# Performance work log

Hardware: AMD Instinct MI355X
Metric: run time of the kernel (lower is better)

## Reference

```python
import jax, jax.numpy as jnp
import numpy as np

B, L, E, H = 32, 2048, 512, 512


def setup_inputs() -> dict:
    key = jax.random.key(0)
    k1, k2, k3, k4 = jax.random.split(key, 4)
    encodings = jax.random.normal(k1, (B, L, E), dtype=jnp.float32)
    lengths = jax.random.randint(k2, (B,), 1, L + 1, dtype=jnp.int32)
    # Glorot-ish scaled params
    W_h = jax.random.normal(k3, (E, H), dtype=jnp.float32) / np.sqrt(E)
    b_h = jnp.zeros((H,), dtype=jnp.float32)
    W_c = jax.random.normal(k4, (H, E), dtype=jnp.float32) / np.sqrt(H)
    return {"encodings": encodings, "lengths": lengths, "W_h": W_h, "b_h": b_h, "W_c": W_c}


def reference(encodings, lengths, W_h, b_h, W_c):
    # encodings: [B, L, E] padded ragged pack; lengths: [B] valid lengths
    mask = jnp.arange(encodings.shape[1])[None, :] < lengths[:, None]  # [B, L]
    # hidden_layer with tanh nonlinearity (TimeDistributedLinear)
    h = jnp.tanh(jnp.einsum('ble,eh->blh', encodings, W_h) + b_h)  # [B, L, H]
    # context_vector (no bias) -> per-feature attention logits [B, L, E]
    att = jnp.einsum('blh,he->ble', h, W_c)
    # timedistributed_softmax: softmax over time axis per sample, per feature
    att = jnp.where(mask[:, :, None], att, -jnp.inf)
    att = jax.nn.softmax(att, axis=1)  # padded positions get weight 0
    # weighted sum over time -> [B, E], then unsqueeze(1)
    out = jnp.sum(att * encodings, axis=1)[:, None, :]  # [B, 1, E]
    return out
```

## Files before the change

kernel.cpp:

```cpp
#include <hip/hip_runtime.h>
#include <math.h>

#define BB 32
#define LL 2048
#define EE 512
#define HH 512

typedef __bf16 bf16_t;
typedef bf16_t bf16x8 __attribute__((ext_vector_type(8)));
typedef float f32x4 __attribute__((ext_vector_type(4)));
typedef unsigned short u16x8 __attribute__((ext_vector_type(8)));

__device__ __forceinline__ unsigned short f2bf(float f) {
  unsigned int u = __builtin_bit_cast(unsigned int, f);
  unsigned int r = (u + 0x7FFFu + ((u >> 16) & 1u)) >> 16;
  return (unsigned short)r;
}
__device__ __forceinline__ float bf2f(unsigned short s) {
  unsigned int u = ((unsigned int)s) << 16;
  return __builtin_bit_cast(float, u);
}
__device__ __forceinline__ bf16x8 ld_frag(const unsigned short* p) {
  u16x8 raw = *(const u16x8*)p;
  return __builtin_bit_cast(bf16x8, raw);
}
__device__ __forceinline__ float tanh_fast(float x) {
  x = fminf(fmaxf(x, -15.f), 15.f);
  float e2 = __expf(2.f * x);
  return (e2 - 1.f) / (e2 + 1.f);
}

__device__ __forceinline__ void frag_issue2(const unsigned short* __restrict__ g,
                                            int k0, bf16x8 f[2]) {
#pragma unroll
  for (int i = 0; i < 2; i++) f[i] = ld_frag(g + (size_t)i * 16 * 512 + k0);
}

#define G1_HALF(F, W, PF) do {                                                  \
    const int k0_ = (((W) + phase) & 15) * 32;                                  \
    const bf16x8 b0_ = ld_frag(&encA[(l15     ) * 520 + k0_ + quad * 8]);       \
    const bf16x8 b1_ = ld_frag(&encA[(16 + l15) * 520 + k0_ + quad * 8]);       \
    const bf16x8 b2_ = ld_frag(&encA[(32 + l15) * 520 + k0_ + quad * 8]);       \
    const bf16x8 b3_ = ld_frag(&encA[(48 + l15) * 520 + k0_ + quad * 8]);       \
    _Pragma("unroll")                                                           \
    for (int t_ = 0; t_ < 2; t_++) {                                            \
      acc[t_ * 4 + 0] = __builtin_amdgcn_mfma_f32_16x16x32_bf16(F[t_], b0_, acc[t_ * 4 + 0], 0, 0, 0); \
      acc[t_ * 4 + 1] = __builtin_amdgcn_mfma_f32_16x16x32_bf16(F[t_], b1_, acc[t_ * 4 + 1], 0, 0, 0); \
      acc[t_ * 4 + 2] = __builtin_amdgcn_mfma_f32_16x16x32_bf16(F[t_], b2_, acc[t_ * 4 + 2], 0, 0, 0); \
      acc[t_ * 4 + 3] = __builtin_amdgcn_mfma_f32_16x16x32_bf16(F[t_], b3_, acc[t_ * 4 + 3], 0, 0, 0); \
    }                                                                           \
    if (PF) frag_issue2(baseW, (((W) + 2 + phase) & 15) * 32, F);               \
  } while (0)

#define G2_HALF(F, W, PF) do {                                                  \
    const int k0_ = (((W) + phase) & 15) * 32;                                  \
    const bf16x8 a0_ = ld_frag(&hS[(l15     ) * 520 + k0_ + quad * 8]);         \
    const bf16x8 a1_ = ld_frag(&hS[(16 + l15) * 520 + k0_ + quad * 8]);         \
    const bf16x8 a2_ = ld_frag(&hS[(32 + l15) * 520 + k0_ + quad * 8]);         \
    const bf16x8 a3_ = ld_frag(&hS[(48 + l15) * 520 + k0_ + quad * 8]);         \
    _Pragma("unroll")                                                           \
    for (int e_ = 0; e_ < 2; e_++) {                                            \
      acc[0 * 2 + e_] = __builtin_amdgcn_mfma_f32_16x16x32_bf16(a0_, F[e_], acc[0 * 2 + e_], 0, 0, 0); \
      acc[1 * 2 + e_] = __builtin_amdgcn_mfma_f32_16x16x32_bf16(a1_, F[e_], acc[1 * 2 + e_], 0, 0, 0); \
      acc[2 * 2 + e_] = __builtin_amdgcn_mfma_f32_16x16x32_bf16(a2_, F[e_], acc[2 * 2 + e_], 0, 0, 0); \
      acc[3 * 2 + e_] = __builtin_amdgcn_mfma_f32_16x16x32_bf16(a3_, F[e_], acc[3 * 2 + e_], 0, 0, 0); \
    }                                                                           \
    if (PF) frag_issue2(baseW, (((W) + 2 + phase) & 15) * 32, F);               \
  } while (0)

__global__ __launch_bounds__(256) void prep_w(
    const float* __restrict__ Wh, const float* __restrict__ Wc,
    unsigned short* __restrict__ WhT, unsigned short* __restrict__ WcT,
    int* __restrict__ q)
{
  if (blockIdx.x == 0 && blockIdx.y == 0 && threadIdx.x == 0) *q = 0;
  const float* src = blockIdx.y ? Wc : Wh;
  unsigned short* dst = blockIdx.y ? WcT : WhT;
  const int tr = (blockIdx.x >> 3) * 64;
  const int tc = (blockIdx.x & 7) * 64;
  const int tid = threadIdx.x;
  __shared__ float tile[64][65];
  for (int i = tid; i < 64 * 16; i += 256) {
    const int r = i >> 4, c4 = (i & 15) << 2;
    const float4 v = *(const float4*)(src + (size_t)(tr + r) * 512 + tc + c4);
    tile[r][c4 + 0] = v.x; tile[r][c4 + 1] = v.y;
    tile[r][c4 + 2] = v.z; tile[r][c4 + 3] = v.w;
  }
  __syncthreads();
  for (int i = tid; i < 64 * 16; i += 256) {
    const int r = i >> 4, c4 = (i & 15) << 2;
    ushort4 pk;
    pk.x = f2bf(tile[c4 + 0][r]); pk.y = f2bf(tile[c4 + 1][r]);
    pk.z = f2bf(tile[c4 + 2][r]); pk.w = f2bf(tile[c4 + 3][r]);
    *(ushort4*)(dst + (size_t)(tc + r) * 512 + tr + c4) = pk;
  }
}

__global__ __launch_bounds__(1024, 1) void attn_main(
    const float* __restrict__ enc, const int* __restrict__ lens,
    const unsigned short* __restrict__ WhT, const float* __restrict__ bh,
    const unsigned short* __restrict__ WcT,
    float* __restrict__ pm, float* __restrict__ ps, float* __restrict__ po,
    int* __restrict__ q, int C, int Lc)
{
  const int tid  = threadIdx.x;
  const int lane = tid & 63;
  const int wave = tid >> 6;
  const int quad = lane >> 4;
  const int l15  = lane & 15;
  const int wbase = wave * 32;

  __shared__ __align__(16) unsigned short encA[64 * 520];
  __shared__ __align__(16) unsigned short hS[64 * 520];
  __shared__ __align__(16) float bhS[512];
  __shared__ int itemS;

  if (tid < 512) bhS[tid] = bh[tid];
  const int nitems = 32 * C;

#pragma unroll 1
  for (;;) {
    __syncthreads();
    if (tid == 0) itemS = atomicAdd(q, 1);
    __syncthreads();
    const int item = itemS;
    if (item >= nitems) break;
    const int b = item & 31;
    const int c = item >> 5;
    const int n = lens[b];
    const int l0 = c * Lc;
    const int nvalid = min(n - l0, Lc);
    if (nvalid <= 0) continue;

    const int phase = (item + wave) & 15;

    float stM[2], stS[2], stO[2];
#pragma unroll
    for (int et = 0; et < 2; et++) { stM[et] = -1e30f; stS[et] = 0.f; stO[et] = 0.f; }

    f32x4 acc[8];

#pragma unroll 1
    for (int r0 = 0; r0 < nvalid; r0 += 64) {
      const float* encRow = enc + ((size_t)b * LL + l0 + r0) * EE;
      for (int i = tid; i < 64 * 128; i += 1024) {
        const int m = i >> 7, e4 = (i & 127) << 2;
        const float4 v = *(const float4*)(encRow + (size_t)m * EE + e4);
        ushort4 pk;
        pk.x = f2bf(v.x); pk.y = f2bf(v.y); pk.z = f2bf(v.z); pk.w = f2bf(v.w);
        *(ushort4*)&encA[m * 520 + e4] = pk;
      }
      __syncthreads();

#pragma unroll
      for (int i = 0; i < 8; i++) acc[i] = (f32x4){0.f, 0.f, 0.f, 0.f};
      {
        const unsigned short* baseW = WhT + (size_t)(wbase + l15) * 512 + quad * 8;
        bf16x8 fA[2], fB[2];
        frag_issue2(baseW, ((0 + phase) & 15) * 32, fA);
        frag_issue2(baseW, ((1 + phase) & 15) * 32, fB);
#pragma unroll 1
        for (int kk = 0; kk < 16; kk += 2) {
          G1_HALF(fA, kk + 0, (kk + 2 < 16));
          G1_HALF(fB, kk + 1, (kk + 3 < 16));
        }
      }

#pragma unroll
      for (int t = 0; t < 2; t++) {
        const f32x4 bv = *(const f32x4*)&bhS[wbase + t * 16 + quad * 4];
#pragma unroll
        for (int mt = 0; mt < 4; mt++) {
          ushort4 pk;
          pk.x = f2bf(tanh_fast(acc[t * 4 + mt][0] + bv[0]));
          pk.y = f2bf(tanh_fast(acc[t * 4 + mt][1] + bv[1]));
          pk.z = f2bf(tanh_fast(acc[t * 4 + mt][2] + bv[2]));
          pk.w = f2bf(tanh_fast(acc[t * 4 + mt][3] + bv[3]));
          *(ushort4*)&hS[(mt * 16 + l15) * 520 + wbase + t * 16 + quad * 4] = pk;
        }
      }
      __syncthreads();

#pragma unroll
      for (int i = 0; i < 8; i++) acc[i] = (f32x4){0.f, 0.f, 0.f, 0.f};
      {
        const unsigned short* baseW = WcT + (size_t)(wbase + l15) * 512 + quad * 8;
        bf16x8 fA[2], fB[2];
        frag_issue2(baseW, ((0 + phase) & 15) * 32, fA);
        frag_issue2(baseW, ((1 + phase) & 15) * 32, fB);
#pragma unroll 1
        for (int kk = 0; kk < 16; kk += 2) {
          G2_HALF(fA, kk + 0, (kk + 2 < 16));
          G2_HALF(fB, kk + 1, (kk + 3 < 16));
        }
      }

#pragma unroll
      for (int et = 0; et < 2; et++) {
        const int e = wbase + et * 16 + l15;
        float lm = -1e30f;
#pragma unroll
        for (int mt = 0; mt < 4; mt++)
#pragma unroll
          for (int r = 0; r < 4; r++) {
            const float vv = (r0 + mt * 16 + quad * 4 + r) < nvalid ? acc[mt * 2 + et][r] : -1e30f;
            lm = fmaxf(lm, vv);
          }
        lm = fmaxf(lm, __shfl_xor(lm, 16));
        lm = fmaxf(lm, __shfl_xor(lm, 32));
        float ls = 0.f, lo = 0.f;
#pragma unroll
        for (int mt = 0; mt < 4; mt++)
#pragma unroll
          for (int r = 0; r < 4; r++) {
            const float vv = (r0 + mt * 16 + quad * 4 + r) < nvalid ? acc[mt * 2 + et][r] : -1e30f;
            const float p  = __expf(vv - lm);
            const float ev = bf2f(encA[(mt * 16 + quad * 4 + r) * 520 + e]);
            ls += p;
            lo += p * ev;
          }
        ls += __shfl_xor(ls, 16); ls += __shfl_xor(ls, 32);
        lo += __shfl_xor(lo, 16); lo += __shfl_xor(lo, 32);
        const float Mn = fmaxf(stM[et], lm);
        const float sc = __expf(stM[et] - Mn);
        const float st = __expf(lm - Mn);
        stS[et] = stS[et] * sc + ls * st;
        stO[et] = stO[et] * sc + lo * st;
        stM[et] = Mn;
      }
      __syncthreads();
    }

    if (quad == 0) {
      const size_t base = ((size_t)b * C + c) * EE;
#pragma unroll
      for (int et = 0; et < 2; et++) {
        const int e = wbase + et * 16 + l15;
        pm[base + e] = stM[et];
        ps[base + e] = stS[et];
        po[base + e] = stO[et];
      }
    }
  }
}

__global__ __launch_bounds__(256) void attn_combine(
    const float* __restrict__ pm, const float* __restrict__ ps,
    const float* __restrict__ po, const int* __restrict__ lens,
    float* __restrict__ out, int C, int Lc)
{
  const int b  = blockIdx.y;
  const int e  = blockIdx.x * 64 + (threadIdx.x & 63);
  const int g  = threadIdx.x >> 6;
  const int n  = lens[b];
  const int cmax = min(C, (n + Lc - 1) / Lc);

  float M = -1e30f, S = 0.f, O = 0.f;
  for (int c = g; c < cmax; c += 4) {
    const size_t base = ((size_t)b * C + c) * EE;
    const float m = pm[base + e];
    const float s = ps[base + e];
    const float o = po[base + e];
    const float Mn  = fmaxf(M, m);
    const float sc0 = __expf(M - Mn);
    const float sc1 = __expf(m - Mn);
    S = S * sc0 + s * sc1;
    O = O * sc0 + o * sc1;
    M = Mn;
  }

  __shared__ float sM[4][64], sS[4][64], sO[4][64];
  sM[g][threadIdx.x & 63] = M;
  sS[g][threadIdx.x & 63] = S;
  sO[g][threadIdx.x & 63] = O;
  __syncthreads();

  if (g == 0) {
    const int le = threadIdx.x & 63;
    float Mt = sM[0][le], St = sS[0][le], Ot = sO[0][le];
#pragma unroll
    for (int gg = 1; gg < 4; gg++) {
      const float m = sM[gg][le];
      const float Mn  = fmaxf(Mt, m);
      const float sc0 = __expf(Mt - Mn);
      const float sc1 = __expf(m - Mn);
      St = St * sc0 + sS[gg][le] * sc1;
      Ot = Ot * sc0 + sO[gg][le] * sc1;
      Mt = Mn;
    }
    out[(size_t)b * EE + e] = Ot / St;
  }
}

extern "C" void kernel_launch(void* const* d_in, const int* in_sizes, int n_in,
                              void* d_out, int out_size, void* d_ws, size_t ws_size,
                              hipStream_t stream) {
  const float* enc  = (const float*)d_in[0];
  const int*   lens = (const int*)d_in[1];
  const float* Wh   = (const float*)d_in[2];
  const float* bh   = (const float*)d_in[3];
  const float* Wc   = (const float*)d_in[4];
  float* out = (float*)d_out;

  const size_t wbytes = (size_t)512 * 512 * sizeof(unsigned short);
  int C = 32;
  while (C > 8 && ws_size < (size_t)3 * BB * C * EE * sizeof(float) + 2 * wbytes + 64)
    C >>= 1;
  const int Lc = LL / C;

  float* pm = (float*)d_ws;
  float* ps = pm + (size_t)BB * C * EE;
  float* po = ps + (size_t)BB * C * EE;
  unsigned short* WhT = (unsigned short*)(po + (size_t)BB * C * EE);
  unsigned short* WcT = WhT + (size_t)512 * 512;
  int* q = (int*)(WcT + (size_t)512 * 512);

  prep_w<<<dim3(64, 2), 256, 0, stream>>>(Wh, Wc, WhT, WcT, q);
  attn_main<<<dim3(256), 1024, 0, stream>>>(enc, lens, WhT, bh, WcT, pm, ps, po, q, C, Lc);
  attn_combine<<<dim3(8, BB), 256, 0, stream>>>(pm, ps, po, lens, out, C, Lc);
}
```

Baseline: 307.3 us.

## Restructure attention kernel: 512-thread blocks, register prefetch of next tile, swizzled LDS, weight slabs

```diff
diff --git a/kernel.cpp b/kernel.cpp
--- a/kernel.cpp
+++ b/kernel.cpp
@@ -5,12 +5,15 @@
 #define LL 2048
 #define EE 512
 #define HH 512
+#define WSL 32
 
 typedef __bf16 bf16_t;
 typedef bf16_t bf16x8 __attribute__((ext_vector_type(8)));
 typedef float f32x4 __attribute__((ext_vector_type(4)));
 typedef unsigned short u16x8 __attribute__((ext_vector_type(8)));
 
+#define MFMA __builtin_amdgcn_mfma_f32_16x16x32_bf16
+
 __device__ __forceinline__ unsigned short f2bf(float f) {
   unsigned int u = __builtin_bit_cast(unsigned int, f);
   unsigned int r = (u + 0x7FFFu + ((u >> 16) & 1u)) >> 16;
@@ -30,42 +33,61 @@
   return (e2 - 1.f) / (e2 + 1.f);
 }
 
-__device__ __forceinline__ void frag_issue2(const unsigned short* __restrict__ g,
-                                            int k0, bf16x8 f[2]) {
-#pragma unroll
-  for (int i = 0; i < 2; i++) f[i] = ld_frag(g + (size_t)i * 16 * 512 + k0);
-}
-
-#define G1_HALF(F, W, PF) do {                                                  \
+__device__ __forceinline__ int swz(int row, int col) {
+  return row * 512 + (col ^ ((row & 7) << 3));
+}
+
+__device__ __forceinline__ void w_issue2(const unsigned short* __restrict__ Wt,
+                                         int rbase, int k0, int lane, u16x8 t[2]) {
+  const unsigned short* g = Wt + (size_t)(rbase + (lane >> 2)) * 512 + k0 + (lane & 3) * 8;
+  t[0] = *(const u16x8*)(g);
+  t[1] = *(const u16x8*)(g + 16 * 512);
+}
+__device__ __forceinline__ void w_write2(unsigned short* buf, int lane, int wslot,
+                                         const u16x8 t[2]) {
+  unsigned short* d = buf + (lane >> 2) * WSL + wslot;
+  *(u16x8*)(d) = t[0];
+  *(u16x8*)(d + 16 * WSL) = t[1];
+}
+
+#define G1_STEP(S, W, PF) do {                                                  \
+    w_write2(slab, lane, wslot, S);                                             \
+    if (PF) w_issue2(WhT, wb, (((W) + 2 + phase) & 15) * 32, lane, S);          \
     const int k0_ = (((W) + phase) & 15) * 32;                                  \
-    const bf16x8 b0_ = ld_frag(&encA[(l15     ) * 520 + k0_ + quad * 8]);       \
-    const bf16x8 b1_ = ld_frag(&encA[(16 + l15) * 520 + k0_ + quad * 8]);       \
-    const bf16x8 b2_ = ld_frag(&encA[(32 + l15) * 520 + k0_ + quad * 8]);       \
-    const bf16x8 b3_ = ld_frag(&encA[(48 + l15) * 520 + k0_ + quad * 8]);       \
-    _Pragma("unroll")                                                           \
-    for (int t_ = 0; t_ < 2; t_++) {                                            \
-      acc[t_ * 4 + 0] = __builtin_amdgcn_mfma_f32_16x16x32_bf16(F[t_], b0_, acc[t_ * 4 + 0], 0, 0, 0); \
-      acc[t_ * 4 + 1] = __builtin_amdgcn_mfma_f32_16x16x32_bf16(F[t_], b1_, acc[t_ * 4 + 1], 0, 0, 0); \
-      acc[t_ * 4 + 2] = __builtin_amdgcn_mfma_f32_16x16x32_bf16(F[t_], b2_, acc[t_ * 4 + 2], 0, 0, 0); \
-      acc[t_ * 4 + 3] = __builtin_amdgcn_mfma_f32_16x16x32_bf16(F[t_], b3_, acc[t_ * 4 + 3], 0, 0, 0); \
-    }                                                                           \
-    if (PF) frag_issue2(baseW, (((W) + 2 + phase) & 15) * 32, F);               \
+    const bf16x8 b0_ = ld_frag(&encA[swz(l15,      k0_ + quad * 8)]);           \
+    const bf16x8 b1_ = ld_frag(&encA[swz(16 + l15, k0_ + quad * 8)]);           \
+    const bf16x8 b2_ = ld_frag(&encA[swz(32 + l15, k0_ + quad * 8)]);           \
+    const bf16x8 b3_ = ld_frag(&encA[swz(48 + l15, k0_ + quad * 8)]);           \
+    const bf16x8 af0_ = ld_frag(&slab[l15 * WSL + rslot]);                      \
+    const bf16x8 af1_ = ld_frag(&slab[(16 + l15) * WSL + rslot]);               \
+    acc[0] = MFMA(af0_, b0_, acc[0], 0, 0, 0);                                  \
+    acc[1] = MFMA(af0_, b1_, acc[1], 0, 0, 0);                                  \
+    acc[2] = MFMA(af0_, b2_, acc[2], 0, 0, 0);                                  \
+    acc[3] = MFMA(af0_, b3_, acc[3], 0, 0, 0);                                  \
+    acc[4] = MFMA(af1_, b0_, acc[4], 0, 0, 0);                                  \
+    acc[5] = MFMA(af1_, b1_, acc[5], 0, 0, 0);                                  \
+    acc[6] = MFMA(af1_, b2_, acc[6], 0, 0, 0);                                  \
+    acc[7] = MFMA(af1_, b3_, acc[7], 0, 0, 0);                                  \
   } while (0)
 
-#define G2_HALF(F, W, PF) do {                                                  \
+#define G2_STEP(S, W, PF) do {                                                  \
+    w_write2(slab, lane, wslot, S);                                             \
+    if (PF) w_issue2(WcT, wb, (((W) + 2 + phase) & 15) * 32, lane, S);          \
     const int k0_ = (((W) + phase) & 15) * 32;                                  \
-    const bf16x8 a0_ = ld_frag(&hS[(l15     ) * 520 + k0_ + quad * 8]);         \
-    const bf16x8 a1_ = ld_frag(&hS[(16 + l15) * 520 + k0_ + quad * 8]);         \
-    const bf16x8 a2_ = ld_frag(&hS[(32 + l15) * 520 + k0_ + quad * 8]);         \
-    const bf16x8 a3_ = ld_frag(&hS[(48 + l15) * 520 + k0_ + quad * 8]);         \
-    _Pragma("unroll")                                                           \
-    for (int e_ = 0; e_ < 2; e_++) {                                            \
-      acc[0 * 2 + e_] = __builtin_amdgcn_mfma_f32_16x16x32_bf16(a0_, F[e_], acc[0 * 2 + e_], 0, 0, 0); \
-      acc[1 * 2 + e_] = __builtin_amdgcn_mfma_f32_16x16x32_bf16(a1_, F[e_], acc[1 * 2 + e_], 0, 0, 0); \
-      acc[2 * 2 + e_] = __builtin_amdgcn_mfma_f32_16x16x32_bf16(a2_, F[e_], acc[2 * 2 + e_], 0, 0, 0); \
-      acc[3 * 2 + e_] = __builtin_amdgcn_mfma_f32_16x16x32_bf16(a3_, F[e_], acc[3 * 2 + e_], 0, 0, 0); \
-    }                                                                           \
-    if (PF) frag_issue2(baseW, (((W) + 2 + phase) & 15) * 32, F);               \
+    const bf16x8 a0_ = ld_frag(&hS[swz(l15,      k0_ + quad * 8)]);             \
+    const bf16x8 a1_ = ld_frag(&hS[swz(16 + l15, k0_ + quad * 8)]);             \
+    const bf16x8 a2_ = ld_frag(&hS[swz(32 + l15, k0_ + quad * 8)]);             \
+    const bf16x8 a3_ = ld_frag(&hS[swz(48 + l15, k0_ + quad * 8)]);             \
+    const bf16x8 cf0_ = ld_frag(&slab[l15 * WSL + rslot]);                      \
+    const bf16x8 cf1_ = ld_frag(&slab[(16 + l15) * WSL + rslot]);               \
+    acc[0] = MFMA(a0_, cf0_, acc[0], 0, 0, 0);                                  \
+    acc[1] = MFMA(a0_, cf1_, acc[1], 0, 0, 0);                                  \
+    acc[2] = MFMA(a1_, cf0_, acc[2], 0, 0, 0);                                  \
+    acc[3] = MFMA(a1_, cf1_, acc[3], 0, 0, 0);                                  \
+    acc[4] = MFMA(a2_, cf0_, acc[4], 0, 0, 0);                                  \
+    acc[5] = MFMA(a2_, cf1_, acc[5], 0, 0, 0);                                  \
+    acc[6] = MFMA(a3_, cf0_, acc[6], 0, 0, 0);                                  \
+    acc[7] = MFMA(a3_, cf1_, acc[7], 0, 0, 0);                                  \
   } while (0)
 
 __global__ __launch_bounds__(256) void prep_w(
@@ -96,7 +118,16 @@
   }
 }
 
-__global__ __launch_bounds__(1024, 1) void attn_main(
+__device__ __forceinline__ int pop_valid(int* q, const int* __restrict__ lens,
+                                         int nitems, int Lc) {
+  int it;
+  for (;;) {
+    it = atomicAdd(q, 1);
+    if (it >= nitems || lens[it & 31] > (it >> 5) * Lc) return it;
+  }
+}
+
+__global__ __launch_bounds__(512, 2) void attn_main(
     const float* __restrict__ enc, const int* __restrict__ lens,
     const unsigned short* __restrict__ WhT, const float* __restrict__ bh,
     const unsigned short* __restrict__ WcT,
@@ -104,71 +135,97 @@
     int* __restrict__ q, int C, int Lc)
 {
   const int tid  = threadIdx.x;
+  const int wave = tid >> 6;
   const int lane = tid & 63;
-  const int wave = tid >> 6;
   const int quad = lane >> 4;
   const int l15  = lane & 15;
-  const int wbase = wave * 32;
-
-  __shared__ __align__(16) unsigned short encA[64 * 520];
-  __shared__ __align__(16) unsigned short hS[64 * 520];
+
+  const int wslot = ((lane & 3) ^ ((lane >> 3) & 3)) * 8;
+  const int rslot = (quad ^ ((l15 >> 1) & 3)) * 8;
+
+  __shared__ __align__(16) unsigned short ebuf[2][64 * 512];
+  __shared__ __align__(16) unsigned short wslabS[8][32 * WSL];
   __shared__ __align__(16) float bhS[512];
   __shared__ int itemS;
 
-  if (tid < 512) bhS[tid] = bh[tid];
+  unsigned short* slab = wslabS[wave];
+  bhS[tid] = bh[tid];
   const int nitems = 32 * C;
+
+  if (tid == 0) itemS = pop_valid(q, lens, nitems, Lc);
+  __syncthreads();
+  int item = itemS;
+  int p = 0;
+
+  float4 eR[8];
+  if (item < nitems) {
+    const float* src = enc + ((size_t)(item & 31) * LL + (size_t)(item >> 5) * Lc) * EE;
+#pragma unroll
+    for (int k = 0; k < 8; k++) {
+      const int i = tid + k * 512;
+      eR[k] = *(const float4*)(src + (size_t)(i >> 7) * EE + ((i & 127) << 2));
+    }
+  }
 
 #pragma unroll 1
   for (;;) {
-    __syncthreads();
-    if (tid == 0) itemS = atomicAdd(q, 1);
-    __syncthreads();
-    const int item = itemS;
     if (item >= nitems) break;
     const int b = item & 31;
     const int c = item >> 5;
-    const int n = lens[b];
     const int l0 = c * Lc;
-    const int nvalid = min(n - l0, Lc);
-    if (nvalid <= 0) continue;
-
+    const int nvalid = min(lens[b] - l0, Lc);
     const int phase = (item + wave) & 15;
-
-    float stM[2], stS[2], stO[2];
-#pragma unroll
-    for (int et = 0; et < 2; et++) { stM[et] = -1e30f; stS[et] = 0.f; stO[et] = 0.f; }
+    unsigned short* encA = ebuf[p];
+    unsigned short* hS   = ebuf[p ^ 1];
+
+#pragma unroll
+    for (int k = 0; k < 8; k++) {
+      const int i = tid + k * 512;
+      ushort4 pk;
+      pk.x = f2bf(eR[k].x); pk.y = f2bf(eR[k].y);
+      pk.z = f2bf(eR[k].z); pk.w = f2bf(eR[k].w);
+      *(ushort4*)&encA[swz(i >> 7, (i & 127) << 2)] = pk;
+    }
+    {
+      const float* encRow = enc + ((size_t)b * LL + l0 + 32) * EE;
+      float4 tmp[8];
+#pragma unroll
+      for (int k = 0; k < 8; k++) {
+        const int i = tid + k * 512;
+        tmp[k] = *(const float4*)(encRow + (size_t)(i >> 7) * EE + ((i & 127) << 2));
+      }
+#pragma unroll
+      for (int k = 0; k < 8; k++) {
+        const int i = tid + k * 512;
+        ushort4 pk;
+        pk.x = f2bf(tmp[k].x); pk.y = f2bf(tmp[k].y);
+        pk.z = f2bf(tmp[k].z); pk.w = f2bf(tmp[k].w);
+        *(ushort4*)&encA[swz(32 + (i >> 7), (i & 127) << 2)] = pk;
+      }
+    }
+    if (tid == 0) itemS = pop_valid(q, lens, nitems, Lc);
+    __syncthreads();
 
     f32x4 acc[8];
 
-#pragma unroll 1
-    for (int r0 = 0; r0 < nvalid; r0 += 64) {
-      const float* encRow = enc + ((size_t)b * LL + l0 + r0) * EE;
-      for (int i = tid; i < 64 * 128; i += 1024) {
-        const int m = i >> 7, e4 = (i & 127) << 2;
-        const float4 v = *(const float4*)(encRow + (size_t)m * EE + e4);
-        ushort4 pk;
-        pk.x = f2bf(v.x); pk.y = f2bf(v.y); pk.z = f2bf(v.z); pk.w = f2bf(v.w);
-        *(ushort4*)&encA[m * 520 + e4] = pk;
-      }
-      __syncthreads();
-
+#pragma unroll
+    for (int h = 0; h < 2; h++) {
+      const int wb = h * 256 + wave * 32;
 #pragma unroll
       for (int i = 0; i < 8; i++) acc[i] = (f32x4){0.f, 0.f, 0.f, 0.f};
       {
-        const unsigned short* baseW = WhT + (size_t)(wbase + l15) * 512 + quad * 8;
-        bf16x8 fA[2], fB[2];
-        frag_issue2(baseW, ((0 + phase) & 15) * 32, fA);
-        frag_issue2(baseW, ((1 + phase) & 15) * 32, fB);
+        u16x8 sA[2], sB[2];
+        w_issue2(WhT, wb, ((0 + phase) & 15) * 32, lane, sA);
+        w_issue2(WhT, wb, ((1 + phase) & 15) * 32, lane, sB);
 #pragma unroll 1
         for (int kk = 0; kk < 16; kk += 2) {
-          G1_HALF(fA, kk + 0, (kk + 2 < 16));
-          G1_HALF(fB, kk + 1, (kk + 3 < 16));
-        }
-      }
-
+          G1_STEP(sA, kk + 0, kk + 2 < 16);
+          G1_STEP(sB, kk + 1, kk + 3 < 16);
+        }
+      }
 #pragma unroll
       for (int t = 0; t < 2; t++) {
-        const f32x4 bv = *(const f32x4*)&bhS[wbase + t * 16 + quad * 4];
+        const f32x4 bv = *(const f32x4*)&bhS[wb + t * 16 + quad * 4];
 #pragma unroll
         for (int mt = 0; mt < 4; mt++) {
           ushort4 pk;
@@ -176,34 +233,49 @@
           pk.y = f2bf(tanh_fast(acc[t * 4 + mt][1] + bv[1]));
           pk.z = f2bf(tanh_fast(acc[t * 4 + mt][2] + bv[2]));
           pk.w = f2bf(tanh_fast(acc[t * 4 + mt][3] + bv[3]));
-          *(ushort4*)&hS[(mt * 16 + l15) * 520 + wbase + t * 16 + quad * 4] = pk;
-        }
-      }
-      __syncthreads();
-
+          *(ushort4*)&hS[swz(mt * 16 + l15, wb + t * 16 + quad * 4)] = pk;
+        }
+      }
+    }
+    __syncthreads();
+
+    int nextItem = nitems;
+    const size_t obase = ((size_t)b * C + c) * EE;
+#pragma unroll
+    for (int h = 0; h < 2; h++) {
+      const int wb = h * 256 + wave * 32;
 #pragma unroll
       for (int i = 0; i < 8; i++) acc[i] = (f32x4){0.f, 0.f, 0.f, 0.f};
       {
-        const unsigned short* baseW = WcT + (size_t)(wbase + l15) * 512 + quad * 8;
-        bf16x8 fA[2], fB[2];
-        frag_issue2(baseW, ((0 + phase) & 15) * 32, fA);
-        frag_issue2(baseW, ((1 + phase) & 15) * 32, fB);
+        u16x8 sA[2], sB[2];
+        w_issue2(WcT, wb, ((0 + phase) & 15) * 32, lane, sA);
+        w_issue2(WcT, wb, ((1 + phase) & 15) * 32, lane, sB);
 #pragma unroll 1
         for (int kk = 0; kk < 16; kk += 2) {
-          G2_HALF(fA, kk + 0, (kk + 2 < 16));
-          G2_HALF(fB, kk + 1, (kk + 3 < 16));
-        }
-      }
-
+          G2_STEP(sA, kk + 0, kk + 2 < 16);
+          G2_STEP(sB, kk + 1, kk + 3 < 16);
+        }
+      }
+      if (h == 1) {
+        nextItem = itemS;
+        if (nextItem < nitems) {
+          const float* src = enc + ((size_t)(nextItem & 31) * LL + (size_t)(nextItem >> 5) * Lc) * EE;
+#pragma unroll
+          for (int k = 0; k < 8; k++) {
+            const int i = tid + k * 512;
+            eR[k] = *(const float4*)(src + (size_t)(i >> 7) * EE + ((i & 127) << 2));
+          }
+        }
+      }
 #pragma unroll
       for (int et = 0; et < 2; et++) {
-        const int e = wbase + et * 16 + l15;
+        const int e = wb + et * 16 + l15;
         float lm = -1e30f;
 #pragma unroll
         for (int mt = 0; mt < 4; mt++)
 #pragma unroll
           for (int r = 0; r < 4; r++) {
-            const float vv = (r0 + mt * 16 + quad * 4 + r) < nvalid ? acc[mt * 2 + et][r] : -1e30f;
+            const float vv = (mt * 16 + quad * 4 + r) < nvalid ? acc[mt * 2 + et][r] : -1e30f;
             lm = fmaxf(lm, vv);
           }
         lm = fmaxf(lm, __shfl_xor(lm, 16));
@@ -213,34 +285,25 @@
         for (int mt = 0; mt < 4; mt++)
 #pragma unroll
           for (int r = 0; r < 4; r++) {
-            const float vv = (r0 + mt * 16 + quad * 4 + r) < nvalid ? acc[mt * 2 + et][r] : -1e30f;
-            const float p  = __expf(vv - lm);
-            const float ev = bf2f(encA[(mt * 16 + quad * 4 + r) * 520 + e]);
-            ls += p;
-            lo += p * ev;
+            const float vv = (mt * 16 + quad * 4 + r) < nvalid ? acc[mt * 2 + et][r] : -1e30f;
+            const float pexp = __expf(vv - lm);
+            const float ev = bf2f(encA[swz(mt * 16 + quad * 4 + r, e)]);
+            ls += pexp;
+            lo += pexp * ev;
           }
         ls += __shfl_xor(ls, 16); ls += __shfl_xor(ls, 32);
         lo += __shfl_xor(lo, 16); lo += __shfl_xor(lo, 32);
-        const float Mn = fmaxf(stM[et], lm);
-        const float sc = __expf(stM[et] - Mn);
-        const float st = __expf(lm - Mn);
-        stS[et] = stS[et] * sc + ls * st;
-        stO[et] = stO[et] * sc + lo * st;
-        stM[et] = Mn;
-      }
-      __syncthreads();
-    }
-
-    if (quad == 0) {
-      const size_t base = ((size_t)b * C + c) * EE;
-#pragma unroll
-      for (int et = 0; et < 2; et++) {
-        const int e = wbase + et * 16 + l15;
-        pm[base + e] = stM[et];
-        ps[base + e] = stS[et];
-        po[base + e] = stO[et];
-      }
-    }
+        if (quad == 0) {
+          pm[obase + e] = lm;
+          ps[obase + e] = ls;
+          po[obase + e] = lo;
+        }
+      }
+    }
+    __syncthreads();
+
+    item = nextItem;
+    p ^= 1;
   }
 }
 
@@ -302,10 +365,7 @@
   const float* Wc   = (const float*)d_in[4];
   float* out = (float*)d_out;
 
-  const size_t wbytes = (size_t)512 * 512 * sizeof(unsigned short);
-  int C = 32;
-  while (C > 8 && ws_size < (size_t)3 * BB * C * EE * sizeof(float) + 2 * wbytes + 64)
-    C >>= 1;
+  const int C = 32;
   const int Lc = LL / C;
 
   float* pm = (float*)d_ws;
@@ -316,6 +376,6 @@
   int* q = (int*)(WcT + (size_t)512 * 512);
 
   prep_w<<<dim3(64, 2), 256, 0, stream>>>(Wh, Wc, WhT, WcT, q);
-  attn_main<<<dim3(256), 1024, 0, stream>>>(enc, lens, WhT, bh, WcT, pm, ps, po, q, C, Lc);
+  attn_main<<<dim3(256), 512, 0, stream>>>(enc, lens, WhT, bh, WcT, pm, ps, po, q, C, Lc);
   attn_combine<<<dim3(8, BB), 256, 0, stream>>>(pm, ps, po, lens, out, C, Lc);
 }
```

After: 260.8 us. 1.18x faster.
